# Performance work log

Hardware: AMD Instinct MI355X
Metric: run time of the kernel (lower is better)

Reference implementation:

```python
import jax, jax.numpy as jnp
import numpy as np

N = 50000      # nodes
E = 800000     # edges (before self loops)
D = 128        # embedding_dimension
HEADS = 4
C = 32         # hidden_channels
NEG_SLOPE = 0.2


def setup_inputs() -> dict:
    key = jax.random.key(0)
    ks = jax.random.split(key, 12)
    s = 0.1
    x = jax.random.normal(ks[0], (N, D), jnp.float32)
    edge_index = jax.random.randint(ks[1], (2, E), 0, N)
    # layer 1: D -> HEADS*C, concat
    W1 = jax.random.normal(ks[2], (D, HEADS * C), jnp.float32) * s
    a_src1 = jax.random.normal(ks[3], (HEADS, C), jnp.float32) * s
    a_dst1 = jax.random.normal(ks[4], (HEADS, C), jnp.float32) * s
    b1 = jnp.zeros((HEADS * C,), jnp.float32)
    # layer 2: HEADS*C -> HEADS*C, concat
    W2 = jax.random.normal(ks[5], (HEADS * C, HEADS * C), jnp.float32) * s
    a_src2 = jax.random.normal(ks[6], (HEADS, C), jnp.float32) * s
    a_dst2 = jax.random.normal(ks[7], (HEADS, C), jnp.float32) * s
    b2 = jnp.zeros((HEADS * C,), jnp.float32)
    # layer 3: HEADS*C -> C, heads=1, no concat (mean over the single head)
    W3 = jax.random.normal(ks[8], (HEADS * C, C), jnp.float32) * s
    a_src3 = jax.random.normal(ks[9], (1, C), jnp.float32) * s
    a_dst3 = jax.random.normal(ks[10], (1, C), jnp.float32) * s
    b3 = jnp.zeros((C,), jnp.float32)
    return {"x": x, "edge_index": edge_index,
            "W1": W1, "a_src1": a_src1, "a_dst1": a_dst1, "b1": b1,
            "W2": W2, "a_src2": a_src2, "a_dst2": a_dst2, "b2": b2,
            "W3": W3, "a_src3": a_src3, "a_dst3": a_dst3, "b3": b3}


def gat_layer(x, src, dst, W, a_s, a_d, b, heads, concat):
    """One PyG-style GATConv (eval mode: dropout inactive).
    x: [N, Fin]; src/dst: [E2] (self loops included)."""
    n = x.shape[0]
    h = (x @ W).reshape(n, heads, -1)                 # [N, H, C]
    alpha_src = (h * a_s).sum(-1)                     # [N, H]
    alpha_dst = (h * a_d).sum(-1)                     # [N, H]
    logits = jax.nn.leaky_relu(alpha_src[src] + alpha_dst[dst], NEG_SLOPE)  # [E2, H]
    # segment softmax over destination nodes
    m = jax.ops.segment_max(logits, dst, num_segments=n)          # [N, H]
    ex = jnp.exp(logits - m[dst])                                  # [E2, H]
    denom = jax.ops.segment_sum(ex, dst, num_segments=n)          # [N, H]
    alpha = ex / (denom[dst] + 1e-16)                              # [E2, H]
    msg = h[src] * alpha[:, :, None]                               # [E2, H, C]
    out = jax.ops.segment_sum(msg, dst, num_segments=n)            # [N, H, C]
    if concat:
        return out.reshape(n, -1) + b
    return out.mean(axis=1) + b


def reference(x, edge_index, W1, a_src1, a_dst1, b1, W2, a_src2, a_dst2, b2,
              W3, a_src3, a_dst3, b3):
    loops = jnp.arange(N, dtype=edge_index.dtype)
    src = jnp.concatenate([edge_index[0], loops])   # add_self_loops=True
    dst = jnp.concatenate([edge_index[1], loops])
    h = gat_layer(x, src, dst, W1, a_src1, a_dst1, b1, HEADS, True)
    h = jax.nn.elu(h)
    h = gat_layer(h, src, dst, W2, a_src2, a_dst2, b2, HEADS, True)
    h = jax.nn.elu(h)
    out = gat_layer(h, src, dst, W3, a_src3, a_dst3, b3, 1, False)
    return out
```

## Files before the change

kernel.cpp:

```cpp
#include <hip/hip_runtime.h>
#include <cmath>

constexpr int NN  = 50000;
constexpr int EE  = 800000;
constexpr int E2C = EE + NN;
constexpr int DIM = 128;

constexpr int NBUCK = 256;
constexpr int BW    = 196;
constexpr int EPT   = 16;
constexpr int CH    = 256 * EPT;
constexpr int NB_B  = (E2C + CH - 1) / CH;
constexpr int CAP   = 4096;
constexpr int SCAP  = 5120;

using bf16x8 = __attribute__((ext_vector_type(8))) short;
using f32x4  = __attribute__((ext_vector_type(4))) float;

__device__ inline unsigned bf16rne(float f) {
    unsigned u = __builtin_bit_cast(unsigned, f);
    return (u + 0x7fffu + ((u >> 16) & 1u)) >> 16;
}
__device__ inline float bflo(unsigned u) { return __builtin_bit_cast(float, u << 16); }
__device__ inline float bfhi(unsigned u) { return __builtin_bit_cast(float, u & 0xffff0000u); }

__global__ __launch_bounds__(256) void cvt_weights(
    const float* __restrict__ W1, const float* __restrict__ W2,
    const float* __restrict__ W3,
    unsigned short* __restrict__ W1t, unsigned short* __restrict__ W2t,
    unsigned short* __restrict__ W3t)
{
    int g = blockIdx.x * 256 + threadIdx.x;
    const float* W; unsigned short* Wt; int cols;
    if (g < 2048)      { W = W1; Wt = W1t; cols = 128; }
    else if (g < 4096) { W = W2; Wt = W2t; cols = 128; g -= 2048; }
    else if (g < 4608) { W = W3; Wt = W3t; cols = 32;  g -= 4096; }
    else return;
    int c  = g / 16;
    int k8 = (g % 16) * 8;
    unsigned up[4];
    #pragma unroll
    for (int j = 0; j < 4; ++j) {
        float a = W[(k8 + 2 * j) * cols + c];
        float b = W[(k8 + 2 * j + 1) * cols + c];
        up[j] = bf16rne(a) | (bf16rne(b) << 16);
    }
    uint4 u; u.x = up[0]; u.y = up[1]; u.z = up[2]; u.w = up[3];
    *(uint4*)(Wt + c * 128 + k8) = u;
}

template<int NT, int NH, bool F32IN>
__global__ __launch_bounds__(256) void gemm_mfma(
    const void* __restrict__ inv, const unsigned short* __restrict__ Wt,
    const float* __restrict__ a_s, const float* __restrict__ a_d,
    unsigned short* __restrict__ hout, float* __restrict__ asrc,
    float* __restrict__ adst)
{
    constexpr int COLS = NT * 16;
    constexpr int TPH  = NT / NH;
    const int lane = threadIdx.x & 63;
    const int wave = threadIdx.x >> 6;
    const int m    = lane & 15;
    const int quad = lane >> 4;
    const int n0   = blockIdx.x * 64 + wave * 16;

    int arow = n0 + m; if (arow >= NN) arow = NN - 1;

    f32x4 acc[NT] = {};
    #pragma unroll
    for (int kq = 0; kq < 4; ++kq) {
        bf16x8 a;
        if constexpr (F32IN) {
            const float* ap = (const float*)inv + (long long)arow * 128 + quad * 8 + kq * 32;
            float4 v0 = *(const float4*)ap;
            float4 v1 = *(const float4*)(ap + 4);
            a[0] = (short)bf16rne(v0.x); a[1] = (short)bf16rne(v0.y);
            a[2] = (short)bf16rne(v0.z); a[3] = (short)bf16rne(v0.w);
            a[4] = (short)bf16rne(v1.x); a[5] = (short)bf16rne(v1.y);
            a[6] = (short)bf16rne(v1.z); a[7] = (short)bf16rne(v1.w);
        } else {
            a = *(const bf16x8*)((const unsigned short*)inv
                    + (long long)arow * 128 + quad * 8 + kq * 32);
        }
        #pragma unroll
        for (int t = 0; t < NT; ++t) {
            bf16x8 b = *(const bf16x8*)(Wt + (t * 16 + m) * 128 + kq * 32 + quad * 8);
            acc[t] = __builtin_amdgcn_mfma_f32_16x16x32_bf16(a, b, acc[t], 0, 0, 0);
        }
    }

    #pragma unroll
    for (int r = 0; r < 4; ++r) {
        int node = n0 + quad * 4 + r;
        if (node < NN) {
            #pragma unroll
            for (int t = 0; t < NT; ++t)
                hout[(long long)node * COLS + t * 16 + m] =
                    (unsigned short)bf16rne(acc[t][r]);
        }
    }

    float asv[NT], adv[NT];
    #pragma unroll
    for (int t = 0; t < NT; ++t) { asv[t] = a_s[t * 16 + m]; adv[t] = a_d[t * 16 + m]; }

    #pragma unroll
    for (int r = 0; r < 4; ++r) {
        const int node = n0 + quad * 4 + r;
        #pragma unroll
        for (int hh = 0; hh < NH; ++hh) {
            float ps = 0.f, pd = 0.f;
            #pragma unroll
            for (int q = 0; q < TPH; ++q) {
                int t = hh * TPH + q;
                ps = fmaf(acc[t][r], asv[t], ps);
                pd = fmaf(acc[t][r], adv[t], pd);
            }
            #pragma unroll
            for (int off = 8; off > 0; off >>= 1) {
                ps += __shfl_down(ps, off, 16);
                pd += __shfl_down(pd, off, 16);
            }
            if (m == 0 && node < NN) {
                asrc[node * NH + hh] = ps;
                adst[node * NH + hh] = pd;
            }
        }
    }

    if (blockIdx.x == 0 && threadIdx.x == 0) {
        #pragma unroll
        for (int hh = 0; hh < NH; ++hh) asrc[NN * NH + hh] = -1e30f;
    }
}

__global__ __launch_bounds__(256) void bucket_bin(
    const int* __restrict__ ei, int* __restrict__ bcursor,
    unsigned* __restrict__ pairs)
{
    __shared__ int cnt[NBUCK];
    __shared__ int scanex[NBUCK];
    __shared__ int base[NBUCK];
    __shared__ int cur[NBUCK];
    __shared__ unsigned stage[CH];

    const int tid = threadIdx.x;
    const long long e0 = (long long)blockIdx.x * CH;
    cnt[tid] = 0;
    __syncthreads();

    unsigned rec[EPT]; int bk[EPT];
    #pragma unroll
    for (int j = 0; j < EPT; ++j) {
        long long e = e0 + tid + j * 256;
        bool valid = e < E2C;
        int ss = 0, dd = 0;
        if (valid) {
            if (e < EE) { ss = ei[e]; dd = ei[EE + e]; }
            else        { ss = dd = (int)(e - EE); }
        }
        int b = dd / BW;
        bk[j]  = valid ? b : -1;
        rec[j] = (unsigned)ss | ((unsigned)(dd - b * BW) << 16) | ((unsigned)b << 24);
        if (valid) atomicAdd(&cnt[b], 1);
    }
    __syncthreads();

    const int myc = cnt[tid];
    scanex[tid] = myc;
    __syncthreads();
    for (int off = 1; off < NBUCK; off <<= 1) {
        int t = (tid >= off) ? scanex[tid - off] : 0;
        __syncthreads();
        scanex[tid] += t;
        __syncthreads();
    }
    int excl = scanex[tid] - myc;
    __syncthreads();
    scanex[tid] = excl;
    cur[tid]    = excl;
    base[tid]   = atomicAdd(&bcursor[tid], myc);
    __syncthreads();

    #pragma unroll
    for (int j = 0; j < EPT; ++j) {
        if (bk[j] >= 0) {
            int p = atomicAdd(&cur[bk[j]], 1);
            stage[p] = rec[j];
        }
    }
    __syncthreads();

    const int total = (e0 + CH <= E2C) ? CH : (int)(E2C - e0);
    for (int j = tid; j < total; j += 256) {
        unsigned p = stage[j];
        int b = (int)(p >> 24);
        pairs[(size_t)b * CAP + base[b] + (j - scanex[b])] = p;
    }
}

__global__ __launch_bounds__(256) void bucket_sort(
    const int* __restrict__ bcursor, const unsigned* __restrict__ pairs,
    int2* __restrict__ rowp, unsigned short* __restrict__ sorted_src)
{
    __shared__ int deg[256];
    __shared__ int scn[256];
    __shared__ int cur[256];
    const int b  = blockIdx.x;
    const int n0 = b * BW;
    const int n1 = (n0 + BW < NN) ? n0 + BW : NN;
    const int nloc = n1 - n0;
    const int tid = threadIdx.x;
    const int mycnt = bcursor[b];
    const unsigned* seg = pairs + (size_t)b * CAP;
    const int base = b * SCAP;

    deg[tid] = 0;
    __syncthreads();
    for (int i = tid; i < mycnt; i += 256)
        atomicAdd(&deg[(seg[i] >> 16) & 0xff], 1);
    __syncthreads();

    const int pv = (deg[tid] + 3) & ~3;
    scn[tid] = pv;
    __syncthreads();
    for (int off = 1; off < 256; off <<= 1) {
        int t = (tid >= off) ? scn[tid - off] : 0;
        __syncthreads();
        scn[tid] += t;
        __syncthreads();
    }
    const int totalp = scn[255];
    const int pexcl  = scn[tid] - pv;
    cur[tid] = base + pexcl;
    if (tid < nloc) rowp[n0 + tid] = make_int2(base + pexcl, base + pexcl + pv);
    __syncthreads();

    for (int i = tid; i < totalp; i += 256)
        sorted_src[base + i] = (unsigned short)NN;
    __syncthreads();
    for (int i = tid; i < mycnt; i += 256) {
        unsigned p = seg[i];
        int pos = atomicAdd(&cur[(p >> 16) & 0xff], 1);
        sorted_src[pos] = (unsigned short)(p & 0xffff);
    }
}

template<int COLS, int NH, bool DO_ELU, bool OUTBF>
__global__ __launch_bounds__(256) void aggr_csr(
    const int2* __restrict__ rowp, const unsigned short* __restrict__ sorted_src,
    const unsigned short* __restrict__ hin,
    const float* __restrict__ asrc, const float* __restrict__ adst,
    const float* __restrict__ bias, void* __restrict__ outv)
{
    constexpr int TPN = COLS / 8;
    constexpr int USTR = COLS / 2;
    int t = blockIdx.x * 256 + threadIdx.x;
    int d = t / TPN;
    int lc = t % TPN;
    if (d >= NN) return;
    const int cc = lc * 8;
    const int head = cc / 32;
    const float ad = adst[d * NH + head];
    const int2 be = rowp[d];
    const int beg = be.x, end = be.y;
    const uint* hp = (const uint*)hin + cc / 2;

    float num[8] = {};
    float den = 0.f;

    ushort4 sv = *(const ushort4*)&sorted_src[beg];
    for (int i = beg; i < end; i += 4) {
        ushort4 nx = *(const ushort4*)&sorted_src[i + 4];
        const int s[4] = {sv.x, sv.y, sv.z, sv.w};
        float a[4];
        uint4 Hv[4];
        #pragma unroll
        for (int j = 0; j < 4; ++j) a[j] = asrc[s[j] * NH + head];
        #pragma unroll
        for (int j = 0; j < 4; ++j)
            Hv[j] = *(const uint4*)&hp[(long long)s[j] * USTR];
        #pragma unroll
        for (int j = 0; j < 4; ++j) {
            float l = a[j] + ad; l = l > 0.f ? l : 0.2f * l;
            float w = __builtin_expf(l);
            den += w;
            num[0] = fmaf(w, bflo(Hv[j].x), num[0]); num[1] = fmaf(w, bfhi(Hv[j].x), num[1]);
            num[2] = fmaf(w, bflo(Hv[j].y), num[2]); num[3] = fmaf(w, bfhi(Hv[j].y), num[3]);
            num[4] = fmaf(w, bflo(Hv[j].z), num[4]); num[5] = fmaf(w, bfhi(Hv[j].z), num[5]);
            num[6] = fmaf(w, bflo(Hv[j].w), num[6]); num[7] = fmaf(w, bfhi(Hv[j].w), num[7]);
        }
        sv = nx;
    }

    float inv = 1.f / (den + 1e-16f);
    float v[8];
    #pragma unroll
    for (int j = 0; j < 8; ++j) {
        v[j] = num[j] * inv + bias[cc + j];
        if (DO_ELU) v[j] = v[j] > 0.f ? v[j] : expm1f(v[j]);
    }
    if constexpr (OUTBF) {
        uint4 u;
        u.x = bf16rne(v[0]) | (bf16rne(v[1]) << 16);
        u.y = bf16rne(v[2]) | (bf16rne(v[3]) << 16);
        u.z = bf16rne(v[4]) | (bf16rne(v[5]) << 16);
        u.w = bf16rne(v[6]) | (bf16rne(v[7]) << 16);
        *(uint4*)((unsigned short*)outv + (long long)d * COLS + cc) = u;
    } else {
        float4 o0 = {v[0], v[1], v[2], v[3]};
        float4 o1 = {v[4], v[5], v[6], v[7]};
        float* out = (float*)outv;
        *(float4*)&out[(long long)d * COLS + cc]     = o0;
        *(float4*)&out[(long long)d * COLS + cc + 4] = o1;
    }
}

extern "C" void kernel_launch(void* const* d_in, const int* in_sizes, int n_in,
                              void* d_out, int out_size, void* d_ws, size_t ws_size,
                              hipStream_t stream)
{
    const float* x   = (const float*)d_in[0];
    const int*   ei  = (const int*)  d_in[1];
    const float* W1  = (const float*)d_in[2];
    const float* as1 = (const float*)d_in[3];
    const float* ad1 = (const float*)d_in[4];
    const float* b1  = (const float*)d_in[5];
    const float* W2  = (const float*)d_in[6];
    const float* as2 = (const float*)d_in[7];
    const float* ad2 = (const float*)d_in[8];
    const float* b2  = (const float*)d_in[9];
    const float* W3  = (const float*)d_in[10];
    const float* as3 = (const float*)d_in[11];
    const float* ad3 = (const float*)d_in[12];
    const float* b3  = (const float*)d_in[13];
    float* out = (float*)d_out;

    unsigned short* H16 = (unsigned short*)d_ws;
    unsigned short* O16 = H16 + (size_t)(NN + 1) * 128;
    unsigned short* P16 = O16 + (size_t)NN * 128;
    unsigned short* W1t = P16 + (size_t)NN * 128;
    unsigned short* W2t = W1t + 128 * 128;
    unsigned short* W3t = W2t + 128 * 128;
    float* ASRC = (float*)(W3t + 32 * 128);
    float* ADST = ASRC + (size_t)(NN + 1) * 4;
    int2* rowp  = (int2*)(ADST + (size_t)NN * 4);
    unsigned short* sorted = (unsigned short*)(rowp + NN);
    int* bcursor = (int*)(sorted + (size_t)NBUCK * SCAP + 8);
    size_t off = ((size_t)(bcursor + NBUCK) - (size_t)d_ws + 15) & ~(size_t)15;
    unsigned* pairs = (unsigned*)((char*)d_ws + off);

    const int gCvtW    = (4608 + 255) / 256;
    const int gGemm    = (NN + 63) / 64;
    const int gAggr128 = (NN * 16 + 255) / 256;
    const int gAggr32  = (NN * 4 + 255) / 256;

    hipMemsetAsync(bcursor, 0, NBUCK * sizeof(int), stream);
    bucket_bin<<<NB_B, 256, 0, stream>>>(ei, bcursor, pairs);
    bucket_sort<<<NBUCK, 256, 0, stream>>>(bcursor, pairs, rowp, sorted);
    cvt_weights<<<gCvtW, 256, 0, stream>>>(W1, W2, W3, W1t, W2t, W3t);

    gemm_mfma<8, 4, true><<<gGemm, 256, 0, stream>>>(x, W1t, as1, ad1, H16, ASRC, ADST);
    aggr_csr<128, 4, true, true><<<gAggr128, 256, 0, stream>>>(
        rowp, sorted, H16, ASRC, ADST, b1, O16);

    gemm_mfma<8, 4, false><<<gGemm, 256, 0, stream>>>(O16, W2t, as2, ad2, H16, ASRC, ADST);
    aggr_csr<128, 4, true, true><<<gAggr128, 256, 0, stream>>>(
        rowp, sorted, H16, ASRC, ADST, b2, P16);

    gemm_mfma<2, 1, false><<<gGemm, 256, 0, stream>>>(P16, W3t, as3, ad3, H16, ASRC, ADST);
    aggr_csr<32, 1, false, false><<<gAggr32, 256, 0, stream>>>(
        rowp, sorted, H16, ASRC, ADST, b3, out);
}
```

Measured before the change: 275.5 us.

## Degree-sort nodes within buckets and widen aggregation to 16 columns per thread

```diff
diff --git a/kernel.cpp b/kernel.cpp
--- a/kernel.cpp
+++ b/kernel.cpp
@@ -8,7 +8,7 @@
 
 constexpr int NBUCK = 256;
 constexpr int BW    = 196;
-constexpr int EPT   = 16;
+constexpr int EPT   = 8;
 constexpr int CH    = 256 * EPT;
 constexpr int NB_B  = (E2C + CH - 1) / CH;
 constexpr int CAP   = 4096;
@@ -28,9 +28,10 @@
     const float* __restrict__ W1, const float* __restrict__ W2,
     const float* __restrict__ W3,
     unsigned short* __restrict__ W1t, unsigned short* __restrict__ W2t,
-    unsigned short* __restrict__ W3t)
+    unsigned short* __restrict__ W3t, int* __restrict__ bcursor)
 {
     int g = blockIdx.x * 256 + threadIdx.x;
+    if (g < NBUCK) bcursor[g] = 0;
     const float* W; unsigned short* Wt; int cols;
     if (g < 2048)      { W = W1; Wt = W1t; cols = 128; }
     else if (g < 4096) { W = W2; Wt = W2t; cols = 128; g -= 2048; }
@@ -201,11 +202,15 @@
 
 __global__ __launch_bounds__(256) void bucket_sort(
     const int* __restrict__ bcursor, const unsigned* __restrict__ pairs,
-    int2* __restrict__ rowp, unsigned short* __restrict__ sorted_src)
+    int2* __restrict__ rowp, unsigned short* __restrict__ sorted_src,
+    unsigned short* __restrict__ perm)
 {
     __shared__ int deg[256];
     __shared__ int scn[256];
     __shared__ int cur[256];
+    __shared__ int hist2[64];
+    __shared__ int scn2[64];
+    __shared__ int cur2[64];
     const int b  = blockIdx.x;
     const int n0 = b * BW;
     const int n1 = (n0 + BW < NN) ? n0 + BW : NN;
@@ -216,13 +221,16 @@
     const int base = b * SCAP;
 
     deg[tid] = 0;
+    if (tid < 64) hist2[tid] = 0;
     __syncthreads();
     for (int i = tid; i < mycnt; i += 256)
         atomicAdd(&deg[(seg[i] >> 16) & 0xff], 1);
     __syncthreads();
 
     const int pv = (deg[tid] + 3) & ~3;
+    int it = pv >> 2; if (it > 63) it = 63;
     scn[tid] = pv;
+    if (tid < nloc) atomicAdd(&hist2[it], 1);
     __syncthreads();
     for (int off = 1; off < 256; off <<= 1) {
         int t = (tid >= off) ? scn[tid - off] : 0;
@@ -230,10 +238,25 @@
         scn[tid] += t;
         __syncthreads();
     }
+    if (tid < 64) scn2[tid] = hist2[tid];
+    __syncthreads();
+    for (int off = 1; off < 64; off <<= 1) {
+        int t = (tid >= off && tid < 64) ? scn2[tid - off] : 0;
+        __syncthreads();
+        if (tid < 64) scn2[tid] += t;
+        __syncthreads();
+    }
+    if (tid < 64) cur2[tid] = scn2[tid] - hist2[tid];
+    __syncthreads();
+
     const int totalp = scn[255];
     const int pexcl  = scn[tid] - pv;
     cur[tid] = base + pexcl;
-    if (tid < nloc) rowp[n0 + tid] = make_int2(base + pexcl, base + pexcl + pv);
+    if (tid < nloc) {
+        int rank = atomicAdd(&cur2[it], 1);
+        perm[n0 + rank] = (unsigned short)(n0 + tid);
+        rowp[n0 + rank] = make_int2(base + pexcl, base + pexcl + pv);
+    }
     __syncthreads();
 
     for (int i = tid; i < totalp; i += 256)
@@ -248,25 +271,27 @@
 
 template<int COLS, int NH, bool DO_ELU, bool OUTBF>
 __global__ __launch_bounds__(256) void aggr_csr(
+    const unsigned short* __restrict__ perm,
     const int2* __restrict__ rowp, const unsigned short* __restrict__ sorted_src,
     const unsigned short* __restrict__ hin,
     const float* __restrict__ asrc, const float* __restrict__ adst,
     const float* __restrict__ bias, void* __restrict__ outv)
 {
-    constexpr int TPN = COLS / 8;
+    constexpr int TPN = COLS / 16;
     constexpr int USTR = COLS / 2;
     int t = blockIdx.x * 256 + threadIdx.x;
-    int d = t / TPN;
+    int rk = t / TPN;
     int lc = t % TPN;
-    if (d >= NN) return;
-    const int cc = lc * 8;
+    if (rk >= NN) return;
+    const int d = perm[rk];
+    const int cc = lc * 16;
     const int head = cc / 32;
     const float ad = adst[d * NH + head];
-    const int2 be = rowp[d];
+    const int2 be = rowp[rk];
     const int beg = be.x, end = be.y;
     const uint* hp = (const uint*)hin + cc / 2;
 
-    float num[8] = {};
+    float num[16] = {};
     float den = 0.f;
 
     ushort4 sv = *(const ushort4*)&sorted_src[beg];
@@ -274,45 +299,61 @@
         ushort4 nx = *(const ushort4*)&sorted_src[i + 4];
         const int s[4] = {sv.x, sv.y, sv.z, sv.w};
         float a[4];
-        uint4 Hv[4];
+        uint4 Hv[4][2];
         #pragma unroll
         for (int j = 0; j < 4; ++j) a[j] = asrc[s[j] * NH + head];
         #pragma unroll
-        for (int j = 0; j < 4; ++j)
-            Hv[j] = *(const uint4*)&hp[(long long)s[j] * USTR];
+        for (int j = 0; j < 4; ++j) {
+            const uint* row = hp + (long long)s[j] * USTR;
+            Hv[j][0] = *(const uint4*)row;
+            Hv[j][1] = *(const uint4*)(row + 4);
+        }
         #pragma unroll
         for (int j = 0; j < 4; ++j) {
             float l = a[j] + ad; l = l > 0.f ? l : 0.2f * l;
             float w = __builtin_expf(l);
             den += w;
-            num[0] = fmaf(w, bflo(Hv[j].x), num[0]); num[1] = fmaf(w, bfhi(Hv[j].x), num[1]);
-            num[2] = fmaf(w, bflo(Hv[j].y), num[2]); num[3] = fmaf(w, bfhi(Hv[j].y), num[3]);
-            num[4] = fmaf(w, bflo(Hv[j].z), num[4]); num[5] = fmaf(w, bfhi(Hv[j].z), num[5]);
-            num[6] = fmaf(w, bflo(Hv[j].w), num[6]); num[7] = fmaf(w, bfhi(Hv[j].w), num[7]);
+            #pragma unroll
+            for (int q = 0; q < 2; ++q) {
+                num[q*8+0] = fmaf(w, bflo(Hv[j][q].x), num[q*8+0]);
+                num[q*8+1] = fmaf(w, bfhi(Hv[j][q].x), num[q*8+1]);
+                num[q*8+2] = fmaf(w, bflo(Hv[j][q].y), num[q*8+2]);
+                num[q*8+3] = fmaf(w, bfhi(Hv[j][q].y), num[q*8+3]);
+                num[q*8+4] = fmaf(w, bflo(Hv[j][q].z), num[q*8+4]);
+                num[q*8+5] = fmaf(w, bfhi(Hv[j][q].z), num[q*8+5]);
+                num[q*8+6] = fmaf(w, bflo(Hv[j][q].w), num[q*8+6]);
+                num[q*8+7] = fmaf(w, bfhi(Hv[j][q].w), num[q*8+7]);
+            }
         }
         sv = nx;
     }
 
     float inv = 1.f / (den + 1e-16f);
-    float v[8];
-    #pragma unroll
-    for (int j = 0; j < 8; ++j) {
+    float v[16];
+    #pragma unroll
+    for (int j = 0; j < 16; ++j) {
         v[j] = num[j] * inv + bias[cc + j];
         if (DO_ELU) v[j] = v[j] > 0.f ? v[j] : expm1f(v[j]);
     }
     if constexpr (OUTBF) {
-        uint4 u;
-        u.x = bf16rne(v[0]) | (bf16rne(v[1]) << 16);
-        u.y = bf16rne(v[2]) | (bf16rne(v[3]) << 16);
-        u.z = bf16rne(v[4]) | (bf16rne(v[5]) << 16);
-        u.w = bf16rne(v[6]) | (bf16rne(v[7]) << 16);
-        *(uint4*)((unsigned short*)outv + (long long)d * COLS + cc) = u;
+        uint4 u0, u1;
+        u0.x = bf16rne(v[0])  | (bf16rne(v[1])  << 16);
+        u0.y = bf16rne(v[2])  | (bf16rne(v[3])  << 16);
+        u0.z = bf16rne(v[4])  | (bf16rne(v[5])  << 16);
+        u0.w = bf16rne(v[6])  | (bf16rne(v[7])  << 16);
+        u1.x = bf16rne(v[8])  | (bf16rne(v[9])  << 16);
+        u1.y = bf16rne(v[10]) | (bf16rne(v[11]) << 16);
+        u1.z = bf16rne(v[12]) | (bf16rne(v[13]) << 16);
+        u1.w = bf16rne(v[14]) | (bf16rne(v[15]) << 16);
+        unsigned short* op = (unsigned short*)outv + (long long)d * COLS + cc;
+        *(uint4*)op       = u0;
+        *(uint4*)(op + 8) = u1;
     } else {
-        float4 o0 = {v[0], v[1], v[2], v[3]};
-        float4 o1 = {v[4], v[5], v[6], v[7]};
-        float* out = (float*)outv;
-        *(float4*)&out[(long long)d * COLS + cc]     = o0;
-        *(float4*)&out[(long long)d * COLS + cc + 4] = o1;
+        float* out = (float*)outv + (long long)d * COLS + cc;
+        *(float4*)(out + 0)  = make_float4(v[0],  v[1],  v[2],  v[3]);
+        *(float4*)(out + 4)  = make_float4(v[4],  v[5],  v[6],  v[7]);
+        *(float4*)(out + 8)  = make_float4(v[8],  v[9],  v[10], v[11]);
+        *(float4*)(out + 12) = make_float4(v[12], v[13], v[14], v[15]);
     }
 }
 
@@ -347,28 +388,28 @@
     int2* rowp  = (int2*)(ADST + (size_t)NN * 4);
     unsigned short* sorted = (unsigned short*)(rowp + NN);
     int* bcursor = (int*)(sorted + (size_t)NBUCK * SCAP + 8);
-    size_t off = ((size_t)(bcursor + NBUCK) - (size_t)d_ws + 15) & ~(size_t)15;
+    unsigned short* perm = (unsigned short*)(bcursor + NBUCK);
+    size_t off = ((size_t)(perm + NN) - (size_t)d_ws + 15) & ~(size_t)15;
     unsigned* pairs = (unsigned*)((char*)d_ws + off);
 
     const int gCvtW    = (4608 + 255) / 256;
     const int gGemm    = (NN + 63) / 64;
-    const int gAggr128 = (NN * 16 + 255) / 256;
-    const int gAggr32  = (NN * 4 + 255) / 256;
-
-    hipMemsetAsync(bcursor, 0, NBUCK * sizeof(int), stream);
+    const int gAggr128 = (NN * 8 + 255) / 256;
+    const int gAggr32  = (NN * 2 + 255) / 256;
+
+    cvt_weights<<<gCvtW, 256, 0, stream>>>(W1, W2, W3, W1t, W2t, W3t, bcursor);
     bucket_bin<<<NB_B, 256, 0, stream>>>(ei, bcursor, pairs);
-    bucket_sort<<<NBUCK, 256, 0, stream>>>(bcursor, pairs, rowp, sorted);
-    cvt_weights<<<gCvtW, 256, 0, stream>>>(W1, W2, W3, W1t, W2t, W3t);
+    bucket_sort<<<NBUCK, 256, 0, stream>>>(bcursor, pairs, rowp, sorted, perm);
 
     gemm_mfma<8, 4, true><<<gGemm, 256, 0, stream>>>(x, W1t, as1, ad1, H16, ASRC, ADST);
     aggr_csr<128, 4, true, true><<<gAggr128, 256, 0, stream>>>(
-        rowp, sorted, H16, ASRC, ADST, b1, O16);
+        perm, rowp, sorted, H16, ASRC, ADST, b1, O16);
 
     gemm_mfma<8, 4, false><<<gGemm, 256, 0, stream>>>(O16, W2t, as2, ad2, H16, ASRC, ADST);
     aggr_csr<128, 4, true, true><<<gAggr128, 256, 0, stream>>>(
-        rowp, sorted, H16, ASRC, ADST, b2, P16);
+        perm, rowp, sorted, H16, ASRC, ADST, b2, P16);
 
     gemm_mfma<2, 1, false><<<gGemm, 256, 0, stream>>>(P16, W3t, as3, ad3, H16, ASRC, ADST);
     aggr_csr<32, 1, false, false><<<gAggr32, 256, 0, stream>>>(
-        rowp, sorted, H16, ASRC, ADST, b3, out);
-}
+        perm, rowp, sorted, H16, ASRC, ADST, b3, out);
+}
```

Result: slower. 286.9 us (+4.1%).

## Fuse bucket sort with first GEMM and fold cursor memset into weight conversion

Applied to the files above, without the earlier changes.

```diff
diff --git a/kernel.cpp b/kernel.cpp
--- a/kernel.cpp
+++ b/kernel.cpp
@@ -4,11 +4,10 @@
 constexpr int NN  = 50000;
 constexpr int EE  = 800000;
 constexpr int E2C = EE + NN;
-constexpr int DIM = 128;
 
 constexpr int NBUCK = 256;
 constexpr int BW    = 196;
-constexpr int EPT   = 16;
+constexpr int EPT   = 8;
 constexpr int CH    = 256 * EPT;
 constexpr int NB_B  = (E2C + CH - 1) / CH;
 constexpr int CAP   = 4096;
@@ -28,9 +27,10 @@
     const float* __restrict__ W1, const float* __restrict__ W2,
     const float* __restrict__ W3,
     unsigned short* __restrict__ W1t, unsigned short* __restrict__ W2t,
-    unsigned short* __restrict__ W3t)
+    unsigned short* __restrict__ W3t, int* __restrict__ bcursor)
 {
     int g = blockIdx.x * 256 + threadIdx.x;
+    if (g < NBUCK) bcursor[g] = 0;
     const float* W; unsigned short* Wt; int cols;
     if (g < 2048)      { W = W1; Wt = W1t; cols = 128; }
     else if (g < 4096) { W = W2; Wt = W2t; cols = 128; g -= 2048; }
@@ -50,8 +50,8 @@
 }
 
 template<int NT, int NH, bool F32IN>
-__global__ __launch_bounds__(256) void gemm_mfma(
-    const void* __restrict__ inv, const unsigned short* __restrict__ Wt,
+__device__ inline void gemm_body(
+    int bid, const void* __restrict__ inv, const unsigned short* __restrict__ Wt,
     const float* __restrict__ a_s, const float* __restrict__ a_d,
     unsigned short* __restrict__ hout, float* __restrict__ asrc,
     float* __restrict__ adst)
@@ -62,7 +62,7 @@
     const int wave = threadIdx.x >> 6;
     const int m    = lane & 15;
     const int quad = lane >> 4;
-    const int n0   = blockIdx.x * 64 + wave * 16;
+    const int n0   = bid * 64 + wave * 16;
 
     int arow = n0 + m; if (arow >= NN) arow = NN - 1;
 
@@ -128,10 +128,20 @@
         }
     }
 
-    if (blockIdx.x == 0 && threadIdx.x == 0) {
+    if (bid == 0 && threadIdx.x == 0) {
         #pragma unroll
         for (int hh = 0; hh < NH; ++hh) asrc[NN * NH + hh] = -1e30f;
     }
+}
+
+template<int NT, int NH, bool F32IN>
+__global__ __launch_bounds__(256) void gemm_mfma(
+    const void* __restrict__ inv, const unsigned short* __restrict__ Wt,
+    const float* __restrict__ a_s, const float* __restrict__ a_d,
+    unsigned short* __restrict__ hout, float* __restrict__ asrc,
+    float* __restrict__ adst)
+{
+    gemm_body<NT, NH, F32IN>(blockIdx.x, inv, Wt, a_s, a_d, hout, asrc, adst);
 }
 
 __global__ __launch_bounds__(256) void bucket_bin(
@@ -199,14 +209,13 @@
     }
 }
 
-__global__ __launch_bounds__(256) void bucket_sort(
-    const int* __restrict__ bcursor, const unsigned* __restrict__ pairs,
+__device__ inline void sort_body(
+    int b, const int* __restrict__ bcursor, const unsigned* __restrict__ pairs,
     int2* __restrict__ rowp, unsigned short* __restrict__ sorted_src)
 {
     __shared__ int deg[256];
     __shared__ int scn[256];
     __shared__ int cur[256];
-    const int b  = blockIdx.x;
     const int n0 = b * BW;
     const int n1 = (n0 + BW < NN) ? n0 + BW : NN;
     const int nloc = n1 - n0;
@@ -236,14 +245,33 @@
     if (tid < nloc) rowp[n0 + tid] = make_int2(base + pexcl, base + pexcl + pv);
     __syncthreads();
 
-    for (int i = tid; i < totalp; i += 256)
+    int lim = totalp + 8; if (lim > SCAP) lim = SCAP;
+    for (int i = tid; i < lim; i += 256)
         sorted_src[base + i] = (unsigned short)NN;
+    if (b == NBUCK - 1 && tid < 8)
+        sorted_src[NBUCK * SCAP + tid] = (unsigned short)NN;
     __syncthreads();
     for (int i = tid; i < mycnt; i += 256) {
         unsigned p = seg[i];
         int pos = atomicAdd(&cur[(p >> 16) & 0xff], 1);
         sorted_src[pos] = (unsigned short)(p & 0xffff);
     }
+}
+
+template<int NT, int NH, bool F32IN>
+__global__ __launch_bounds__(256) void sort_gemm(
+    const int* __restrict__ bcursor, const unsigned* __restrict__ pairs,
+    int2* __restrict__ rowp, unsigned short* __restrict__ sorted_src,
+    const void* __restrict__ inv, const unsigned short* __restrict__ Wt,
+    const float* __restrict__ a_s, const float* __restrict__ a_d,
+    unsigned short* __restrict__ hout, float* __restrict__ asrc,
+    float* __restrict__ adst)
+{
+    if (blockIdx.x < NBUCK)
+        sort_body(blockIdx.x, bcursor, pairs, rowp, sorted_src);
+    else
+        gemm_body<NT, NH, F32IN>(blockIdx.x - NBUCK, inv, Wt, a_s, a_d,
+                                 hout, asrc, adst);
 }
 
 template<int COLS, int NH, bool DO_ELU, bool OUTBF>
@@ -352,15 +380,15 @@
 
     const int gCvtW    = (4608 + 255) / 256;
     const int gGemm    = (NN + 63) / 64;
+    const int gSortG   = NBUCK + gGemm;
     const int gAggr128 = (NN * 16 + 255) / 256;
     const int gAggr32  = (NN * 4 + 255) / 256;
 
-    hipMemsetAsync(bcursor, 0, NBUCK * sizeof(int), stream);
+    cvt_weights<<<gCvtW, 256, 0, stream>>>(W1, W2, W3, W1t, W2t, W3t, bcursor);
     bucket_bin<<<NB_B, 256, 0, stream>>>(ei, bcursor, pairs);
-    bucket_sort<<<NBUCK, 256, 0, stream>>>(bcursor, pairs, rowp, sorted);
-    cvt_weights<<<gCvtW, 256, 0, stream>>>(W1, W2, W3, W1t, W2t, W3t);
-
-    gemm_mfma<8, 4, true><<<gGemm, 256, 0, stream>>>(x, W1t, as1, ad1, H16, ASRC, ADST);
+
+    sort_gemm<8, 4, true><<<gSortG, 256, 0, stream>>>(
+        bcursor, pairs, rowp, sorted, x, W1t, as1, ad1, H16, ASRC, ADST);
     aggr_csr<128, 4, true, true><<<gAggr128, 256, 0, stream>>>(
         rowp, sorted, H16, ASRC, ADST, b1, O16);
 
```

Result: no change. 271.6 us (-1.4%).
